# Performance work log

Hardware: AMD Instinct MI355X
Metric: run time of the kernel (lower is better)

Reference implementation:

```python
import jax, jax.numpy as jnp
import numpy as np

B, IN, H = 8192, 1024, 1024


def setup_inputs() -> dict:
    key = jax.random.key(0)
    ks = jax.random.split(key, 20)
    std = 1.0 / np.sqrt(H)
    u = lambda k, shape: jax.random.uniform(k, shape, jnp.float32, -std, std)
    inp = {
        "x": jax.random.normal(ks[0], (B, IN), jnp.float32),
        "hx": jax.random.normal(ks[1], (B, H), jnp.float32),
        "cx": jax.random.normal(ks[2], (B, H), jnp.float32),
        "task_id": 0,
        # x2h weights [H, IN] (torch Linear layout) and biases [H]
        "wxi": u(ks[3], (H, IN)), "bxi": u(ks[4], (H,)),
        "wxf": u(ks[5], (H, IN)), "bxf": u(ks[6], (H,)),
        "wxc": u(ks[7], (H, IN)), "bxc": u(ks[8], (H,)),
        "wxo": u(ks[9], (H, IN)), "bxo": u(ks[10], (H,)),
        # h2h weights [H, H] and biases [H]
        "whi": u(ks[11], (H, H)), "bhi": u(ks[12], (H,)),
        "whf": u(ks[13], (H, H)), "bhf": u(ks[14], (H,)),
        "whc": u(ks[15], (H, H)), "bhc": u(ks[16], (H,)),
        "who": u(ks[17], (H, H)), "bho": u(ks[18], (H,)),
    }
    return inp


def reference(x, hx, cx, task_id,
              wxi, bxi, wxf, bxf, wxc, bxc, wxo, bxo,
              whi, bhi, whf, bhf, whc, bhc, who, bho):
    # x = x.view(-1, x.size(1)) is identity for 2D input
    # gate pre-activations: Linear(x) + Linear(hx)  (torch: x @ W.T + b)
    ingate = x @ wxi.T + bxi + hx @ whi.T + bhi
    forgetgate = x @ wxf.T + bxf + hx @ whf.T + bhf
    cellgate = x @ wxc.T + bxc + hx @ whc.T + bhc
    outgate = x @ wxo.T + bxo + hx @ who.T + bho

    i = jax.nn.sigmoid(ingate)
    f = jax.nn.sigmoid(forgetgate)
    g = jnp.tanh(cellgate)
    o = jax.nn.sigmoid(outgate)

    cy = cx * f + i * g
    hy = o * jnp.tanh(cy)
    return hy, cy
```

## Files before the change

kernel.cpp:

```cpp
#include <hip/hip_runtime.h>
#include <hip/hip_bf16.h>

#define B_DIM  8192
#define IN_DIM 1024
#define H_DIM  1024
#define K_DIM  2048
#define NT     (K_DIM / 64)

typedef __attribute__((ext_vector_type(8))) short bf16x8;
typedef __attribute__((ext_vector_type(4))) float f32x4;

__device__ __forceinline__ void mfma_16x16x32_bf16(f32x4& d, const bf16x8& a, const bf16x8& b) {
  asm("v_mfma_f32_16x16x32_bf16 %0, %1, %2, %0" : "+v"(d) : "v"(a), "v"(b));
}

__device__ __forceinline__ void gload16(const void* g, void* l) {
  __builtin_amdgcn_global_load_lds(
      (const __attribute__((address_space(1))) void*)g,
      (__attribute__((address_space(3))) void*)l,
      16, 0, 0);
}

__device__ __forceinline__ float fast_sigmoid(float x) {
  return 1.0f / (1.0f + __expf(-x));
}
__device__ __forceinline__ float fast_tanh(float x) {
  float e = __expf(2.0f * x);
  return 1.0f - 2.0f / (e + 1.0f);
}

__global__ __launch_bounds__(256) void pack_a_kernel(
    const float* __restrict__ x, const float* __restrict__ hx,
    __hip_bfloat16* __restrict__ A) {
  const int idx = blockIdx.x * 256 + threadIdx.x;
  const int r  = idx >> 8;
  const int kk = (idx & 255) << 3;
  const float* src = (kk < IN_DIM) ? (x + (size_t)r * IN_DIM + kk)
                                   : (hx + (size_t)r * H_DIM + (kk - IN_DIM));
  const float4 v0 = ((const float4*)src)[0];
  const float4 v1 = ((const float4*)src)[1];
  __hip_bfloat16 t[8];
  t[0] = __float2bfloat16(v0.x); t[1] = __float2bfloat16(v0.y);
  t[2] = __float2bfloat16(v0.z); t[3] = __float2bfloat16(v0.w);
  t[4] = __float2bfloat16(v1.x); t[5] = __float2bfloat16(v1.y);
  t[6] = __float2bfloat16(v1.z); t[7] = __float2bfloat16(v1.w);
  *(uint4*)(A + ((size_t)idx << 3)) = *(const uint4*)t;
}

__global__ __launch_bounds__(256) void pack_w_kernel(
    const float* __restrict__ wxi, const float* __restrict__ wxf,
    const float* __restrict__ wxc, const float* __restrict__ wxo,
    const float* __restrict__ whi, const float* __restrict__ whf,
    const float* __restrict__ whc, const float* __restrict__ who,
    __hip_bfloat16* __restrict__ W) {
  const int idx = blockIdx.x * 256 + threadIdx.x;
  const int row = idx >> 8;
  const int kk  = (idx & 255) << 3;
  const int g = row >> 10, n = row & 1023;
  const float* src;
  if (kk < IN_DIM) {
    const float* p = (g == 0) ? wxi : (g == 1) ? wxf : (g == 2) ? wxc : wxo;
    src = p + (size_t)n * IN_DIM + kk;
  } else {
    const float* p = (g == 0) ? whi : (g == 1) ? whf : (g == 2) ? whc : who;
    src = p + (size_t)n * H_DIM + (kk - IN_DIM);
  }
  const float4 v0 = ((const float4*)src)[0];
  const float4 v1 = ((const float4*)src)[1];
  __hip_bfloat16 t[8];
  t[0] = __float2bfloat16(v0.x); t[1] = __float2bfloat16(v0.y);
  t[2] = __float2bfloat16(v0.z); t[3] = __float2bfloat16(v0.w);
  t[4] = __float2bfloat16(v1.x); t[5] = __float2bfloat16(v1.y);
  t[6] = __float2bfloat16(v1.z); t[7] = __float2bfloat16(v1.w);
  *(uint4*)(W + ((size_t)idx << 3)) = *(const uint4*)t;
}


template<int MH>
__device__ __forceinline__ void load_af(const __hip_bfloat16 (*sAp)[64],
                                        bf16x8 (&af)[4][2], int arowbase,
                                        int chk0, int chk1) {
#pragma unroll
  for (int m = 0; m < 4; ++m) {
    const int row = arowbase + (MH * 4 + m) * 16;
    af[m][0] = *(const bf16x8*)&sAp[row][chk0];
    af[m][1] = *(const bf16x8*)&sAp[row][chk1];
  }
}

template<int GH>
__device__ __forceinline__ void load_bf(const __hip_bfloat16 (*sWp)[64][64],
                                        bf16x8 (&bf)[2][2], int wrow,
                                        int chk0, int chk1) {
#pragma unroll
  for (int gi = 0; gi < 2; ++gi) {
    bf[gi][0] = *(const bf16x8*)&sWp[GH * 2 + gi][wrow][chk0];
    bf[gi][1] = *(const bf16x8*)&sWp[GH * 2 + gi][wrow][chk1];
  }
}

template<int MH, int GH>
__device__ __forceinline__ void mfma16(f32x4 (&acc)[4][8],
                                       const bf16x8 (&af)[4][2],
                                       const bf16x8 (&bf)[2][2]) {
  __builtin_amdgcn_s_setprio(1);
#pragma unroll
  for (int gi = 0; gi < 2; ++gi)
#pragma unroll
    for (int m = 0; m < 4; ++m) {
      mfma_16x16x32_bf16(acc[GH * 2 + gi][MH * 4 + m], af[m][0], bf[gi][0]);
      mfma_16x16x32_bf16(acc[GH * 2 + gi][MH * 4 + m], af[m][1], bf[gi][1]);
    }
  __builtin_amdgcn_s_setprio(0);
}

__global__ __launch_bounds__(512, 2) void lstm_gemm_kernel(
    const __hip_bfloat16* __restrict__ A,
    const __hip_bfloat16* __restrict__ W,
    const float* __restrict__ cx,
    const float* __restrict__ bxi, const float* __restrict__ bhi,
    const float* __restrict__ bxf, const float* __restrict__ bhf,
    const float* __restrict__ bxc, const float* __restrict__ bhc,
    const float* __restrict__ bxo, const float* __restrict__ bho,
    float* __restrict__ hy, float* __restrict__ cy) {

  __shared__ __align__(16) __hip_bfloat16 sA[2][256][64];
  __shared__ __align__(16) __hip_bfloat16 sW[2][4][64][64];

  const int tid  = threadIdx.x;
  const int w    = tid >> 6;
  const int lane = tid & 63;
  const int wm = w >> 2, wn = w & 3;
  const int lq = lane >> 4, lr16 = lane & 15;

  const int bid = blockIdx.x;
  const int swz = (bid & 7) * 64 + (bid >> 3);
  const int row0 = (swz >> 4) * 256;
  const int col0 = (swz & 15) * 64;

  const int srow = tid >> 3;
  const int scs  = (tid & 7) ^ (srow & 7);
  const __hip_bfloat16* Asrc = A + (size_t)(row0 + srow) * K_DIM + scs * 8;
  const __hip_bfloat16* Wsrc = W + (size_t)(col0 + srow) * K_DIM + scs * 8;
  const size_t Wg = (size_t)H_DIM * K_DIM;

  const int chk0 = ((lq)     ^ (lr16 & 7)) * 8;
  const int chk1 = ((4 + lq) ^ (lr16 & 7)) * 8;
  const int arowbase = wm * 128 + lr16;
  const int wrow = wn * 16 + lr16;

  f32x4 acc[4][8];
#pragma unroll
  for (int g = 0; g < 4; ++g)
#pragma unroll
    for (int m = 0; m < 8; ++m)
      acc[g][m] = (f32x4){0.f, 0.f, 0.f, 0.f};

#define ISSUE_A4(P, KT)                                                        \
  {                                                                            \
    const size_t kof = (size_t)(KT) * 64;                                      \
    gload16(Asrc + (size_t)0 * 64 * K_DIM + kof, (char*)&sA[P][0][0]   + tid * 16); \
    gload16(Asrc + (size_t)1 * 64 * K_DIM + kof, (char*)&sA[P][64][0]  + tid * 16); \
    gload16(Asrc + (size_t)2 * 64 * K_DIM + kof, (char*)&sA[P][128][0] + tid * 16); \
    gload16(Asrc + (size_t)3 * 64 * K_DIM + kof, (char*)&sA[P][192][0] + tid * 16); \
  }
#define ISSUE_W4(P, KT)                                                        \
  {                                                                            \
    const size_t kof = (size_t)(KT) * 64;                                      \
    gload16(Wsrc + (size_t)0 * Wg + kof, (char*)&sW[P][0][0][0] + tid * 16);   \
    gload16(Wsrc + (size_t)1 * Wg + kof, (char*)&sW[P][1][0][0] + tid * 16);   \
    gload16(Wsrc + (size_t)2 * Wg + kof, (char*)&sW[P][2][0][0] + tid * 16);   \
    gload16(Wsrc + (size_t)3 * Wg + kof, (char*)&sW[P][3][0][0] + tid * 16);   \
  }

  ISSUE_A4(0, 0);
  ISSUE_W4(0, 0);

  bf16x8 af[4][2];
  bf16x8 bf[2][2];

  for (int t = 0; t < NT; ++t) {
    const int p = t & 1, q = p ^ 1;
    const int tn = (t + 1 < NT) ? t + 1 : NT - 1;
    const __hip_bfloat16(*sAp)[64] = sA[p];
    const __hip_bfloat16(*sWp)[64][64] = sW[p];

    ISSUE_A4(q, tn);
    asm volatile("s_waitcnt vmcnt(4)\n\ts_barrier" ::: "memory");
    load_af<0>(sAp, af, arowbase, chk0, chk1);
    load_bf<0>(sWp, bf, wrow, chk0, chk1);
    mfma16<0, 0>(acc, af, bf);
    __builtin_amdgcn_s_barrier();

    ISSUE_W4(q, tn);
    load_bf<1>(sWp, bf, wrow, chk0, chk1);
    mfma16<0, 1>(acc, af, bf);
    __builtin_amdgcn_s_barrier();

    load_af<1>(sAp, af, arowbase, chk0, chk1);
    mfma16<1, 1>(acc, af, bf);
    __builtin_amdgcn_s_barrier();

    load_bf<0>(sWp, bf, wrow, chk0, chk1);
    mfma16<1, 0>(acc, af, bf);
    __builtin_amdgcn_s_barrier();
  }

  const int h = col0 + wrow;
  const float bi = bxi[h] + bhi[h];
  const float bff = bxf[h] + bhf[h];
  const float bc = bxc[h] + bhc[h];
  const float bo = bxo[h] + bho[h];
#pragma unroll
  for (int m = 0; m < 8; ++m) {
#pragma unroll
    for (int j = 0; j < 4; ++j) {
      const int r = row0 + wm * 128 + m * 16 + lq * 4 + j;
      const size_t o = (size_t)r * H_DIM + h;
      const float ig = fast_sigmoid(acc[0][m][j] + bi);
      const float fg = fast_sigmoid(acc[1][m][j] + bff);
      const float gg = fast_tanh   (acc[2][m][j] + bc);
      const float og = fast_sigmoid(acc[3][m][j] + bo);
      const float c  = cx[o] * fg + ig * gg;
      cy[o] = c;
      hy[o] = og * fast_tanh(c);
    }
  }
#undef ISSUE_A4
#undef ISSUE_W4
}

extern "C" void kernel_launch(void* const* d_in, const int* in_sizes, int n_in,
                              void* d_out, int out_size, void* d_ws, size_t ws_size,
                              hipStream_t stream) {
  const float* x   = (const float*)d_in[0];
  const float* hx  = (const float*)d_in[1];
  const float* cx  = (const float*)d_in[2];
  const float* wxi = (const float*)d_in[4];  const float* bxi = (const float*)d_in[5];
  const float* wxf = (const float*)d_in[6];  const float* bxf = (const float*)d_in[7];
  const float* wxc = (const float*)d_in[8];  const float* bxc = (const float*)d_in[9];
  const float* wxo = (const float*)d_in[10]; const float* bxo = (const float*)d_in[11];
  const float* whi = (const float*)d_in[12]; const float* bhi = (const float*)d_in[13];
  const float* whf = (const float*)d_in[14]; const float* bhf = (const float*)d_in[15];
  const float* whc = (const float*)d_in[16]; const float* bhc = (const float*)d_in[17];
  const float* who = (const float*)d_in[18]; const float* bho = (const float*)d_in[19];

  __hip_bfloat16* Abf = (__hip_bfloat16*)d_ws;
  __hip_bfloat16* Wbf = (__hip_bfloat16*)((char*)d_ws + (size_t)B_DIM * K_DIM * 2);

  float* hy  = (float*)d_out;
  float* cyo = (float*)d_out + (size_t)B_DIM * H_DIM;

  pack_a_kernel<<<(B_DIM * K_DIM / 8) / 256, 256, 0, stream>>>(x, hx, Abf);
  pack_w_kernel<<<(4 * H_DIM * K_DIM / 8) / 256, 256, 0, stream>>>(
      wxi, wxf, wxc, wxo, whi, whf, whc, who, Wbf);

  lstm_gemm_kernel<<<dim3(512), 512, 0, stream>>>(
      Abf, Wbf, cx, bxi, bhi, bxf, bhf, bxc, bhc, bxo, bho, hy, cyo);
}
```

Measured before the change: 183.1 us.

## Restructure GEMM main loop to prefetch A two tiles ahead with split W fragments

Rewrites the main loop so the A tile is staged two K-steps ahead and the W tile one step ahead, using a unified byte-addressed LDS buffer. Two W fragment sets are kept in registers so each gate pair is loaded once per tile, and phases are reordered so global loads land during MFMA work. Block-to-tile mapping also changes so each XCD owns two column tiles across all row tiles, aiming at better L2 reuse of weights. The cost is more live registers and more complex barrier and vmcnt bookkeeping that could race on buffer reuse.

Measured after the change: 169.8 us. 1.08x faster.

```diff
diff --git a/kernel.cpp b/kernel.cpp
--- a/kernel.cpp
+++ b/kernel.cpp
@@ -5,7 +5,8 @@
 #define IN_DIM 1024
 #define H_DIM  1024
 #define K_DIM  2048
-#define NT     (K_DIM / 64)
+#define BK     64
+#define NT     (K_DIM / BK)
 
 typedef __attribute__((ext_vector_type(8))) short bf16x8;
 typedef __attribute__((ext_vector_type(4))) float f32x4;
@@ -75,45 +76,6 @@
   *(uint4*)(W + ((size_t)idx << 3)) = *(const uint4*)t;
 }
 
-
-template<int MH>
-__device__ __forceinline__ void load_af(const __hip_bfloat16 (*sAp)[64],
-                                        bf16x8 (&af)[4][2], int arowbase,
-                                        int chk0, int chk1) {
-#pragma unroll
-  for (int m = 0; m < 4; ++m) {
-    const int row = arowbase + (MH * 4 + m) * 16;
-    af[m][0] = *(const bf16x8*)&sAp[row][chk0];
-    af[m][1] = *(const bf16x8*)&sAp[row][chk1];
-  }
-}
-
-template<int GH>
-__device__ __forceinline__ void load_bf(const __hip_bfloat16 (*sWp)[64][64],
-                                        bf16x8 (&bf)[2][2], int wrow,
-                                        int chk0, int chk1) {
-#pragma unroll
-  for (int gi = 0; gi < 2; ++gi) {
-    bf[gi][0] = *(const bf16x8*)&sWp[GH * 2 + gi][wrow][chk0];
-    bf[gi][1] = *(const bf16x8*)&sWp[GH * 2 + gi][wrow][chk1];
-  }
-}
-
-template<int MH, int GH>
-__device__ __forceinline__ void mfma16(f32x4 (&acc)[4][8],
-                                       const bf16x8 (&af)[4][2],
-                                       const bf16x8 (&bf)[2][2]) {
-  __builtin_amdgcn_s_setprio(1);
-#pragma unroll
-  for (int gi = 0; gi < 2; ++gi)
-#pragma unroll
-    for (int m = 0; m < 4; ++m) {
-      mfma_16x16x32_bf16(acc[GH * 2 + gi][MH * 4 + m], af[m][0], bf[gi][0]);
-      mfma_16x16x32_bf16(acc[GH * 2 + gi][MH * 4 + m], af[m][1], bf[gi][1]);
-    }
-  __builtin_amdgcn_s_setprio(0);
-}
-
 __global__ __launch_bounds__(512, 2) void lstm_gemm_kernel(
     const __hip_bfloat16* __restrict__ A,
     const __hip_bfloat16* __restrict__ W,
@@ -124,8 +86,7 @@
     const float* __restrict__ bxo, const float* __restrict__ bho,
     float* __restrict__ hy, float* __restrict__ cy) {
 
-  __shared__ __align__(16) __hip_bfloat16 sA[2][256][64];
-  __shared__ __align__(16) __hip_bfloat16 sW[2][4][64][64];
+  __shared__ __align__(16) char lds[2][64 * 1024];
 
   const int tid  = threadIdx.x;
   const int w    = tid >> 6;
@@ -134,9 +95,11 @@
   const int lq = lane >> 4, lr16 = lane & 15;
 
   const int bid = blockIdx.x;
-  const int swz = (bid & 7) * 64 + (bid >> 3);
-  const int row0 = (swz >> 4) * 256;
-  const int col0 = (swz & 15) * 64;
+  const int xcd = bid & 7, idx = bid >> 3;
+  const int col_tile = xcd * 2 + (idx >> 5);
+  const int row_tile = idx & 31;
+  const int row0 = row_tile * 256;
+  const int col0 = col_tile * 64;
 
   const int srow = tid >> 3;
   const int scs  = (tid & 7) ^ (srow & 7);
@@ -144,10 +107,11 @@
   const __hip_bfloat16* Wsrc = W + (size_t)(col0 + srow) * K_DIM + scs * 8;
   const size_t Wg = (size_t)H_DIM * K_DIM;
 
-  const int chk0 = ((lq)     ^ (lr16 & 7)) * 8;
-  const int chk1 = ((4 + lq) ^ (lr16 & 7)) * 8;
-  const int arowbase = wm * 128 + lr16;
-  const int wrow = wn * 16 + lr16;
+  const int xr = lr16 & 7;
+  const int aoff0 = wm * 16384 + lr16 * 128 + ((lq)     ^ xr) * 16;
+  const int aoff1 = wm * 16384 + lr16 * 128 + ((4 + lq) ^ xr) * 16;
+  const int woff0 = 32768 + (wn * 16 + lr16) * 128 + ((lq)     ^ xr) * 16;
+  const int woff1 = 32768 + (wn * 16 + lr16) * 128 + ((4 + lq) ^ xr) * 16;
 
   f32x4 acc[4][8];
 #pragma unroll
@@ -156,61 +120,115 @@
     for (int m = 0; m < 8; ++m)
       acc[g][m] = (f32x4){0.f, 0.f, 0.f, 0.f};
 
-#define ISSUE_A4(P, KT)                                                        \
-  {                                                                            \
-    const size_t kof = (size_t)(KT) * 64;                                      \
-    gload16(Asrc + (size_t)0 * 64 * K_DIM + kof, (char*)&sA[P][0][0]   + tid * 16); \
-    gload16(Asrc + (size_t)1 * 64 * K_DIM + kof, (char*)&sA[P][64][0]  + tid * 16); \
-    gload16(Asrc + (size_t)2 * 64 * K_DIM + kof, (char*)&sA[P][128][0] + tid * 16); \
-    gload16(Asrc + (size_t)3 * 64 * K_DIM + kof, (char*)&sA[P][192][0] + tid * 16); \
-  }
-#define ISSUE_W4(P, KT)                                                        \
-  {                                                                            \
-    const size_t kof = (size_t)(KT) * 64;                                      \
-    gload16(Wsrc + (size_t)0 * Wg + kof, (char*)&sW[P][0][0][0] + tid * 16);   \
-    gload16(Wsrc + (size_t)1 * Wg + kof, (char*)&sW[P][1][0][0] + tid * 16);   \
-    gload16(Wsrc + (size_t)2 * Wg + kof, (char*)&sW[P][2][0][0] + tid * 16);   \
-    gload16(Wsrc + (size_t)3 * Wg + kof, (char*)&sW[P][3][0][0] + tid * 16);   \
-  }
-
-  ISSUE_A4(0, 0);
-  ISSUE_W4(0, 0);
-
-  bf16x8 af[4][2];
-  bf16x8 bf[2][2];
+#define STAGE_A(Q, KT)                                                        \
+  {                                                                           \
+    const size_t kof = (size_t)(KT) * BK;                                     \
+    gload16(Asrc + kof,                 &lds[Q][tid * 16]);                   \
+    gload16(Asrc + 64 * K_DIM + kof,    &lds[Q][8192  + tid * 16]);           \
+    gload16(Asrc + 128 * K_DIM + kof,   &lds[Q][16384 + tid * 16]);           \
+    gload16(Asrc + 192 * K_DIM + kof,   &lds[Q][24576 + tid * 16]);           \
+  }
+#define STAGE_W(Q, KT)                                                        \
+  {                                                                           \
+    const size_t kof = (size_t)(KT) * BK;                                     \
+    gload16(Wsrc + kof,          &lds[Q][32768 + tid * 16]);                  \
+    gload16(Wsrc + Wg + kof,     &lds[Q][40960 + tid * 16]);                  \
+    gload16(Wsrc + 2 * Wg + kof, &lds[Q][49152 + tid * 16]);                  \
+    gload16(Wsrc + 3 * Wg + kof, &lds[Q][57344 + tid * 16]);                  \
+  }
+#define BAR()  asm volatile("s_barrier" ::: "memory")
+
+  STAGE_A(0, 0);
+  STAGE_W(0, 0);
+  STAGE_A(1, 1);
+  asm volatile("s_waitcnt vmcnt(4)\n\ts_barrier" ::: "memory");
+
+  bf16x8 af[4][2], wf0[2][2], wf1[2][2];
 
   for (int t = 0; t < NT; ++t) {
     const int p = t & 1, q = p ^ 1;
-    const int tn = (t + 1 < NT) ? t + 1 : NT - 1;
-    const __hip_bfloat16(*sAp)[64] = sA[p];
-    const __hip_bfloat16(*sWp)[64][64] = sW[p];
-
-    ISSUE_A4(q, tn);
+    const int tn1 = (t + 1 < NT) ? t + 1 : NT - 1;
+    const int tn2 = (t + 2 < NT) ? t + 2 : NT - 1;
+    const char* rb = lds[p];
+
+#pragma unroll
+    for (int m = 0; m < 4; ++m) {
+      af[m][0] = *(const bf16x8*)(rb + aoff0 + m * 2048);
+      af[m][1] = *(const bf16x8*)(rb + aoff1 + m * 2048);
+    }
+#pragma unroll
+    for (int gi = 0; gi < 2; ++gi) {
+      wf0[gi][0] = *(const bf16x8*)(rb + woff0 + gi * 8192);
+      wf0[gi][1] = *(const bf16x8*)(rb + woff1 + gi * 8192);
+    }
+    STAGE_W(q, tn1);
+    BAR();
+    __builtin_amdgcn_s_setprio(1);
+#pragma unroll
+    for (int gi = 0; gi < 2; ++gi)
+#pragma unroll
+      for (int m = 0; m < 4; ++m) {
+        mfma_16x16x32_bf16(acc[gi][m], af[m][0], wf0[gi][0]);
+        mfma_16x16x32_bf16(acc[gi][m], af[m][1], wf0[gi][1]);
+      }
+    __builtin_amdgcn_s_setprio(0);
+    BAR();
+
+#pragma unroll
+    for (int gi = 0; gi < 2; ++gi) {
+      wf1[gi][0] = *(const bf16x8*)(rb + woff0 + (2 + gi) * 8192);
+      wf1[gi][1] = *(const bf16x8*)(rb + woff1 + (2 + gi) * 8192);
+    }
+    BAR();
+    __builtin_amdgcn_s_setprio(1);
+#pragma unroll
+    for (int gi = 0; gi < 2; ++gi)
+#pragma unroll
+      for (int m = 0; m < 4; ++m) {
+        mfma_16x16x32_bf16(acc[2 + gi][m], af[m][0], wf1[gi][0]);
+        mfma_16x16x32_bf16(acc[2 + gi][m], af[m][1], wf1[gi][1]);
+      }
+    __builtin_amdgcn_s_setprio(0);
+    BAR();
+
+#pragma unroll
+    for (int m = 0; m < 4; ++m) {
+      af[m][0] = *(const bf16x8*)(rb + aoff0 + 8192 + m * 2048);
+      af[m][1] = *(const bf16x8*)(rb + aoff1 + 8192 + m * 2048);
+    }
+    BAR();
+    __builtin_amdgcn_s_setprio(1);
+#pragma unroll
+    for (int gi = 0; gi < 2; ++gi)
+#pragma unroll
+      for (int m = 0; m < 4; ++m) {
+        mfma_16x16x32_bf16(acc[2 + gi][4 + m], af[m][0], wf1[gi][0]);
+        mfma_16x16x32_bf16(acc[2 + gi][4 + m], af[m][1], wf1[gi][1]);
+      }
+    __builtin_amdgcn_s_setprio(0);
+    BAR();
+
+    STAGE_A(p, tn2);
     asm volatile("s_waitcnt vmcnt(4)\n\ts_barrier" ::: "memory");
-    load_af<0>(sAp, af, arowbase, chk0, chk1);
-    load_bf<0>(sWp, bf, wrow, chk0, chk1);
-    mfma16<0, 0>(acc, af, bf);
-    __builtin_amdgcn_s_barrier();
-
-    ISSUE_W4(q, tn);
-    load_bf<1>(sWp, bf, wrow, chk0, chk1);
-    mfma16<0, 1>(acc, af, bf);
-    __builtin_amdgcn_s_barrier();
-
-    load_af<1>(sAp, af, arowbase, chk0, chk1);
-    mfma16<1, 1>(acc, af, bf);
-    __builtin_amdgcn_s_barrier();
-
-    load_bf<0>(sWp, bf, wrow, chk0, chk1);
-    mfma16<1, 0>(acc, af, bf);
-    __builtin_amdgcn_s_barrier();
-  }
-
-  const int h = col0 + wrow;
-  const float bi = bxi[h] + bhi[h];
+    __builtin_amdgcn_s_setprio(1);
+#pragma unroll
+    for (int gi = 0; gi < 2; ++gi)
+#pragma unroll
+      for (int m = 0; m < 4; ++m) {
+        mfma_16x16x32_bf16(acc[gi][4 + m], af[m][0], wf0[gi][0]);
+        mfma_16x16x32_bf16(acc[gi][4 + m], af[m][1], wf0[gi][1]);
+      }
+    __builtin_amdgcn_s_setprio(0);
+    BAR();
+  }
+
+  asm volatile("s_waitcnt vmcnt(0)" ::: "memory");
+
+  const int h = col0 + wn * 16 + lr16;
+  const float bi  = bxi[h] + bhi[h];
   const float bff = bxf[h] + bhf[h];
-  const float bc = bxc[h] + bhc[h];
-  const float bo = bxo[h] + bho[h];
+  const float bc  = bxc[h] + bhc[h];
+  const float bo  = bxo[h] + bho[h];
 #pragma unroll
   for (int m = 0; m < 8; ++m) {
 #pragma unroll
@@ -226,8 +244,9 @@
       hy[o] = og * fast_tanh(c);
     }
   }
-#undef ISSUE_A4
-#undef ISSUE_W4
+#undef STAGE_A
+#undef STAGE_W
+#undef BAR
 }
 
 extern "C" void kernel_launch(void* const* d_in, const int* in_sizes, int n_in,
```
